# Optimization experiments

Measured on AMD Instinct MI355X. Metric: run time of the kernel, lower is better.

Reference implementation:

```python
import jax, jax.numpy as jnp
from jax import lax
import numpy as np

N_FFT = 1024
HOP = 256
CUTOFF = N_FFT // 2 + 1  # 513


def _make_bases():
    n = np.arange(N_FFT)
    # periodic hann window (scipy get_window('hann', N, fftbins=True))
    win = 0.5 - 0.5 * np.cos(2.0 * np.pi * n / N_FFT)
    fb = np.fft.fft(np.eye(N_FFT))
    FB = np.vstack([fb[:CUTOFF].real, fb[:CUTOFF].imag])  # [1026, 1024]
    scale = N_FFT / HOP
    fwd = (FB * win[None, :]).astype(np.float32)                      # [1026, 1024]
    inv = (np.linalg.pinv(scale * FB).T * win[None, :]).astype(np.float32)  # [1026, 1024]
    win_sq = (win ** 2).astype(np.float32)
    return jnp.asarray(fwd), jnp.asarray(inv), jnp.asarray(win_sq)

FWD_BASIS, INV_BASIS, WIN_SQ = _make_bases()


def setup_inputs() -> dict:
    key = jax.random.key(0)
    k1, k2 = jax.random.split(key)
    audio = jax.random.normal(k1, (4, 1048576), dtype=jnp.float32)
    bias_spec = jax.random.uniform(k2, (1, CUTOFF, 1), dtype=jnp.float32)
    return {"audio": audio, "bias_spec": bias_spec}


def reference(audio, bias_spec):
    strength = 0.1
    pad = N_FFT // 2
    # ---- STFT.transform: reflect pad + strided conv1d with fourier basis ----
    x = jnp.pad(audio, ((0, 0), (pad, pad)), mode='reflect')[:, None, :]  # [B,1,T+N]
    ft = lax.conv_general_dilated(
        x, FWD_BASIS[:, None, :], window_strides=(HOP,), padding='VALID',
        dimension_numbers=('NCH', 'OIH', 'NCH'))  # [B, 1026, F]
    re, im = ft[:, :CUTOFF, :], ft[:, CUTOFF:, :]
    mag = jnp.sqrt(re * re + im * im)
    phase = jnp.arctan2(im, re)
    # ---- denoise: bias subtract + clamp ----
    mag_d = jnp.maximum(mag - bias_spec * strength, 0.0)
    # ---- STFT.inverse: cos/sin recombine + conv_transpose1d ----
    rec = jnp.concatenate([mag_d * jnp.cos(phase), mag_d * jnp.sin(phase)], axis=1)  # [B,1026,F]
    # conv_transpose1d(stride=HOP) == dilated conv with flipped, channel-swapped kernel
    K = jnp.flip(INV_BASIS, axis=-1)[None, :, :]  # OIH: [1, 1026, 1024]
    inv = lax.conv_general_dilated(
        rec, K, window_strides=(1,), padding=[(N_FFT - 1, N_FFT - 1)],
        lhs_dilation=(HOP,), dimension_numbers=('NCH', 'OIH', 'NCH'))  # [B,1,(F-1)*HOP+N]
    # ---- window_sumsquare (vectorized overlap-add of win_sq) ----
    F = mag.shape[-1]
    n_len = N_FFT + HOP * (F - 1)
    idx = (jnp.arange(F)[:, None] * HOP + jnp.arange(N_FFT)[None, :]).reshape(-1)
    ws = jnp.zeros((n_len,), jnp.float32).at[idx].add(jnp.tile(WIN_SQ, F))
    tiny = jnp.finfo(jnp.float32).tiny
    inv = jnp.where(ws > tiny, inv / ws, inv) * (float(N_FFT) / HOP)
    # trim filter_length/2 from both ends
    return inv[:, :, pad:-pad]
```

## Files before the change

kernel.cpp:

```cpp
#include <hip/hip_runtime.h>
#include <math.h>


#define NFFT 1024
#define HOP  256
#define CUT  513
#define NB   4
#define LAUD 1048576
#define NFR  4097
#define NSEG 4224
#define NZROW 4100
#define NCOL 4096
#define ABLEN 1082368

typedef __attribute__((ext_vector_type(4))) float f32x4;
typedef __attribute__((ext_vector_type(8))) short bf16x8;

#define AS1 __attribute__((address_space(1)))
#define AS3 __attribute__((address_space(3)))

__device__ __forceinline__ unsigned short f2bf(float x) {
    unsigned u = __float_as_uint(x);
    u += 0x7FFF + ((u >> 16) & 1);
    return (unsigned short)(u >> 16);
}
__device__ __forceinline__ float bf2f(unsigned short h) {
    return __uint_as_float(((unsigned)h) << 16);
}

__global__ __launch_bounds__(256) void build_bases_k(
    ushort* __restrict__ fwdT, ushort* __restrict__ invT2) {
    __shared__ float ctab[1024];
    const int tid = threadIdx.x, bx = blockIdx.x;
    const float CST = 6.135923151542565e-3f;
    #pragma unroll
    for (int i = 0; i < 4; ++i) ctab[(i << 8) + tid] = cosf(CST * (float)((i << 8) + tid));
    __syncthreads();
    int idx = (bx << 8) + tid;
    {
        int ch = idx >> 8, h = idx & 255;
        int k = (ch < CUT) ? ch : ch - 512;
        int m = (k * h) & 1023;
        float base = (ch < CUT) ? ctab[m] : -ctab[(m + 768) & 1023];
        fwdT[idx] = f2bf(base);
    }
    {
        int h = idx >> 10, ch = idx & 1023;
        int k = (ch < CUT) ? ch : ch - 512;
        int m = (k * h) & 1023;
        float base = (ch < CUT) ? ctab[m] : -ctab[(m + 768) & 1023];
        float d = (k == 0 || k == 512) ? (1.0f / 1024.0f) : (2.0f / 1024.0f);
        invT2[idx] = f2bf(base * d);
    }
}

__global__ void cvt_audio_k(const float* __restrict__ audio, ushort* __restrict__ aud) {
    const int NV = ABLEN / 8;
    int idx = blockIdx.x * blockDim.x + threadIdx.x;
    if (idx >= NB * NV) return;
    int b = idx / NV;
    int t8 = (idx - b * NV) << 3;
    const float* ap = audio + (long)b * LAUD;
    ushort o[8];
    int j0 = t8 - 512;
    if (j0 >= 0 && j0 + 7 < LAUD) {
        f32x4 v0 = *(const f32x4*)(ap + j0);
        f32x4 v1 = *(const f32x4*)(ap + j0 + 4);
        #pragma unroll
        for (int q = 0; q < 4; ++q) { o[q] = f2bf(v0[q]); o[4 + q] = f2bf(v1[q]); }
    } else {
        #pragma unroll
        for (int q = 0; q < 8; ++q) {
            int t = t8 + q;
            float v = 0.f;
            if (t < LAUD + 1024) {
                int j = t - 512;
                if (j < 0) j = -j;
                if (j >= LAUD) j = 2 * LAUD - 2 - j;
                v = ap[j];
            }
            o[q] = f2bf(v);
        }
    }
    *(ushort4*)(aud + (long)b * ABLEN + t8)     = *(ushort4*)&o[0];
    *(ushort4*)(aud + (long)b * ABLEN + t8 + 4) = *(ushort4*)&o[4];
}

__global__ __launch_bounds__(256) void gemm_t_k(
    const ushort* __restrict__ fwdT, const ushort* __restrict__ aud,
    ushort* __restrict__ T) {
    __shared__ char smem[32768];
    const int tid = threadIdx.x;
    const int wid = tid >> 6, lane = tid & 63;
    const int lh = lane & 15, lg = lane >> 4;
    const int wm = wid >> 1, wn = wid & 1;
    int w = (blockIdx.x & 7) * 132 + (blockIdx.x >> 3);
    const int f0 = (w % 33) << 7;
    const int c0 = ((w / 33) & 7) << 7;
    const int b  = w / 264;
    const ushort* ab = aud + (long)b * ABLEN;
    f32x4 acc[4][4] = {};

    for (int k0 = 0; k0 < 256; k0 += 64) {
        if (k0) __syncthreads();
        #pragma unroll
        for (int i = 0; i < 4; ++i) {
            int ci = (i << 8) + tid;
            int row = ci >> 3;
            int ks = k0 + (((ci & 7) ^ (row & 7)) << 3);
            __builtin_amdgcn_global_load_lds(
                (const AS1 unsigned int*)(fwdT + ((c0 + row) << 8) + ks),
                (AS3 unsigned int*)(smem + (i << 12) + (wid << 10)), 16, 0, 0);
            __builtin_amdgcn_global_load_lds(
                (const AS1 unsigned int*)(ab + (f0 + row) * 256 + ks),
                (AS3 unsigned int*)(smem + 16384 + (i << 12) + (wid << 10)), 16, 0, 0);
        }
        __syncthreads();
        #pragma unroll
        for (int s = 0; s < 2; ++s) {
            bf16x8 av[4], bv[4];
            #pragma unroll
            for (int i = 0; i < 4; ++i) {
                int r = (wm << 6) + (i << 4) + lh;
                av[i] = *(const bf16x8*)(smem + (r << 7) + ((((s << 2) + lg) ^ (r & 7)) << 4));
                int q = (wn << 6) + (i << 4) + lh;
                bv[i] = *(const bf16x8*)(smem + 16384 + (q << 7) + ((((s << 2) + lg) ^ (q & 7)) << 4));
            }
            #pragma unroll
            for (int i = 0; i < 4; ++i)
                #pragma unroll
                for (int j = 0; j < 4; ++j)
                    acc[i][j] = __builtin_amdgcn_mfma_f32_16x16x32_bf16(av[i], bv[j], acc[i][j], 0, 0, 0);
        }
    }
    ushort* Tb = T + (long)b * NSEG * 1024;
    #pragma unroll
    for (int i = 0; i < 4; ++i) {
        int c = c0 + (wm << 6) + (i << 4) + (lg << 2);
        #pragma unroll
        for (int j = 0; j < 4; ++j) {
            int g = f0 + (wn << 6) + (j << 4) + lh;
            ushort4 o;
            o.x = f2bf(acc[i][j][0]); o.y = f2bf(acc[i][j][1]);
            o.z = f2bf(acc[i][j][2]); o.w = f2bf(acc[i][j][3]);
            *(ushort4*)(Tb + ((long)g << 10) + c) = o;
        }
    }
}

__global__ __launch_bounds__(256) void elem_a_k(
    const ushort* __restrict__ T, const float* __restrict__ bias,
    ushort* __restrict__ Z) {
    __shared__ ushort Tl[4096];
    __shared__ float Xr[513], Xi[513];
    __shared__ float Zr_[513], Zi_[513];
    int bid = blockIdx.x;
    int b = bid / NFR, f = bid - b * NFR;
    const ushort* Tr = T + ((long)(b * NSEG + f) << 10);
    ushort* Zo = Z + ((long)(b * NZROW + f) << 10);
    const int tid = threadIdx.x;

    ((uint4*)Tl)[tid]       = ((const uint4*)Tr)[tid];
    ((uint4*)Tl)[tid + 256] = ((const uint4*)Tr)[tid + 256];
    __syncthreads();

    #pragma unroll
    for (int half = 0; half < 2; ++half) {
        int k = (half << 8) + tid;
        if (k > 512) continue;
        float a[4], bb[4];
        #pragma unroll
        for (int d = 0; d < 4; ++d) {
            a[d]  = bf2f(Tl[(d << 10) + k]);
            bb[d] = (k >= 1 && k <= 511) ? bf2f(Tl[(d << 10) + 512 + k]) : 0.f;
        }
        int r = k & 3;
        float xr, xi;
        if      (r == 0) { xr = a[0] + a[1] + a[2] + a[3];   xi = bb[0] + bb[1] + bb[2] + bb[3]; }
        else if (r == 1) { xr = a[0] + bb[1] - a[2] - bb[3]; xi = bb[0] - a[1] - bb[2] + a[3]; }
        else if (r == 2) { xr = a[0] - a[1] + a[2] - a[3];   xi = bb[0] - bb[1] + bb[2] - bb[3]; }
        else             { xr = a[0] - bb[1] - a[2] + bb[3]; xi = bb[0] + a[1] - bb[2] - a[3]; }
        Xr[k] = xr; Xi[k] = xi;
    }
    if (tid == 0) {
        float a[4];
        #pragma unroll
        for (int d = 0; d < 4; ++d) a[d] = bf2f(Tl[(d << 10) + 512]);
        Xr[512] = a[0] - a[1] + a[2] - a[3];
        Xr[512] = a[0] + a[1] + a[2] + a[3];
        Xi[512] = 0.f;
    }
    __syncthreads();

    #pragma unroll
    for (int half = 0; half < 3; ++half) {
        int k = (half < 2) ? (half << 8) + tid : 512;
        if (half == 2 && tid != 0) continue;
        if (k > 512) continue;
        int km = k - 1, kp = k + 1;
        float smr, smi, spr, spi;
        if (km < 0) { smr = Xr[1];  smi = -Xi[1]; }  else { smr = Xr[km]; smi = Xi[km]; }
        if (kp > 512) { spr = Xr[511]; spi = -Xi[511]; } else { spr = Xr[kp]; spi = Xi[kp]; }
        float xwr = 0.5f * Xr[k] - 0.25f * (smr + spr);
        float xwi = 0.5f * Xi[k] - 0.25f * (smi + spi);
        float mag = sqrtf(xwr * xwr + xwi * xwi);
        float s = mag > 0.f ? fmaxf(mag - 0.1f * bias[k], 0.f) / mag : 0.f;
        Zr_[k] = xwr * s; Zi_[k] = xwi * s;
    }
    __syncthreads();

    #pragma unroll
    for (int half = 0; half < 3; ++half) {
        int k = (half < 2) ? (half << 8) + tid : 512;
        if (half == 2 && tid != 0) continue;
        if (k > 512) continue;
        int km = k - 1, kp = k + 1;
        float smr, smi, spr, spi;
        if (km < 0) { smr = Zr_[1];  smi = -Zi_[1]; }  else { smr = Zr_[km]; smi = Zi_[km]; }
        if (kp > 512) { spr = Zr_[511]; spi = -Zi_[511]; } else { spr = Zr_[kp]; spi = Zi_[kp]; }
        float zr = 0.5f * Zr_[k] - 0.25f * (smr + spr);
        float zi = 0.5f * Zi_[k] - 0.25f * (smi + spi);
        Zo[k] = f2bf(zr);
        if (k >= 1 && k <= 511) Zo[512 + k] = f2bf(zi);
    }
}

__global__ __launch_bounds__(256) void elem_b_k(
    const ushort* __restrict__ Z, ushort* __restrict__ C) {
    __shared__ ushort Zl[4096];
    int bid = blockIdx.x;
    int b = bid >> 12, j = bid & 4095;
    int g = j + 2;
    const ushort* Zb = Z + (long)b * NZROW * 1024;
    ushort* Cr = C + ((long)(b * NCOL + j) << 10);
    const int tid = threadIdx.x;
    const int f0 = g - 3;

    #pragma unroll
    for (int v = 0; v < 2; ++v) {
        int idx = (v << 8) + tid;
        int row = idx >> 7;
        int f = f0 + row;
        uint4 val = make_uint4(0, 0, 0, 0);
        if (f >= 0 && f < NFR)
            val = ((const uint4*)(Zb + ((long)f << 10)))[idx & 127];
        ((uint4*)Zl)[idx] = val;
    }
    __syncthreads();

    #pragma unroll
    for (int half = 0; half < 3; ++half) {
        int k = (half < 2) ? (half << 8) + tid : 512;
        if (half == 2 && tid != 0) continue;
        if (k > 512) continue;
        int r = k & 3;
        float cr = 0.f, ci = 0.f;
        #pragma unroll
        for (int d = 0; d < 4; ++d) {
            int row = 3 - d;
            float zr = bf2f(Zl[(row << 10) + k]);
            float zi = (k >= 1 && k <= 511) ? bf2f(Zl[(row << 10) + 512 + k]) : 0.f;
            int rd = (d * r) & 3;
            if      (rd == 0) { cr += zr; ci += zi; }
            else if (rd == 1) { cr -= zi; ci += zr; }
            else if (rd == 2) { cr -= zr; ci -= zi; }
            else              { cr += zi; ci -= zr; }
        }
        Cr[k] = f2bf(cr);
        if (k >= 1 && k <= 511) Cr[512 + k] = f2bf(ci);
    }
}

__global__ __launch_bounds__(512) void gemm_c_k(
    const ushort* __restrict__ invT2, const ushort* __restrict__ C,
    float* __restrict__ out) {
    __shared__ char smem[49152];
    const int tid = threadIdx.x;
    const int wid = tid >> 6, lane = tid & 63;
    const int lh = lane & 15, lg = lane >> 4;
    const int g = wid >> 2;
    const int wid2 = wid & 3;
    const int wm = wid2 >> 1, wn = wid2 & 1;
    const int tg = tid & 255;
    int w = (blockIdx.x & 7) * 64 + (blockIdx.x >> 3);
    const int h0  = (w & 1) << 7;
    const int j0  = ((w >> 1) & 63) << 6;
    const int fo0 = 2 + j0;
    const int b   = w >> 7;
    const ushort* Cb = C + (long)b * NCOL * 1024;
    char* sm = smem + g * 24576;
    f32x4 acc[4][2] = {};

    for (int k0s = 0; k0s < 512; k0s += 64) {
        if (k0s) __syncthreads();
        int kk = (g << 9) + k0s;
        #pragma unroll
        for (int i = 0; i < 4; ++i) {
            int ci = (i << 8) + tg;
            int row = ci >> 3;
            int swz = (((ci & 7) ^ (row & 7)) << 3);
            __builtin_amdgcn_global_load_lds(
                (const AS1 unsigned int*)(invT2 + ((h0 + row) << 10) + kk + swz),
                (AS3 unsigned int*)(sm + (i << 12) + (wid2 << 10)), 16, 0, 0);
        }
        #pragma unroll
        for (int i = 0; i < 2; ++i) {
            int ci = (i << 8) + tg;
            int row = ci >> 3;
            int swz = (((ci & 7) ^ (row & 7)) << 3);
            __builtin_amdgcn_global_load_lds(
                (const AS1 unsigned int*)(Cb + ((long)(j0 + row) << 10) + kk + swz),
                (AS3 unsigned int*)(sm + 16384 + (i << 12) + (wid2 << 10)), 16, 0, 0);
        }
        __syncthreads();
        #pragma unroll
        for (int s = 0; s < 2; ++s) {
            bf16x8 av[4], bv[2];
            #pragma unroll
            for (int i = 0; i < 4; ++i) {
                int r = (wm << 6) + (i << 4) + lh;
                av[i] = *(const bf16x8*)(sm + (r << 7) + ((((s << 2) + lg) ^ (r & 7)) << 4));
            }
            #pragma unroll
            for (int j = 0; j < 2; ++j) {
                int rq = (wn << 5) + (j << 4) + lh;
                bv[j] = *(const bf16x8*)(sm + 16384 + (rq << 7) + ((((s << 2) + lg) ^ (rq & 7)) << 4));
            }
            #pragma unroll
            for (int i = 0; i < 4; ++i)
                #pragma unroll
                for (int j = 0; j < 2; ++j)
                    acc[i][j] = __builtin_amdgcn_mfma_f32_16x16x32_bf16(av[i], bv[j], acc[i][j], 0, 0, 0);
        }
    }
    __syncthreads();
    float* red = (float*)smem;
    if (g == 1) {
        #pragma unroll
        for (int i = 0; i < 4; ++i)
            #pragma unroll
            for (int j = 0; j < 2; ++j) {
                int hl = (wm << 6) + (i << 4) + (lg << 2);
                int fl = (wn << 5) + (j << 4) + lh;
                #pragma unroll
                for (int q = 0; q < 4; ++q)
                    red[(hl + q) * 64 + fl] = acc[i][j][q];
            }
    }
    __syncthreads();
    if (g == 1) return;
    float* ob = out + (long)b * LAUD;
    const float CST = 6.135923151542565e-3f;
    #pragma unroll
    for (int i = 0; i < 4; ++i) {
        int hbase = h0 + (wm << 6) + (i << 4) + (lg << 2);
        int hl = (wm << 6) + (i << 4) + (lg << 2);
        #pragma unroll
        for (int j = 0; j < 2; ++j) {
            int fo = fo0 + (wn << 5) + (j << 4) + lh;
            int fl = (wn << 5) + (j << 4) + lh;
            f32x4 v = acc[i][j];
            #pragma unroll
            for (int q = 0; q < 4; ++q) v[q] += red[(hl + q) * 64 + fl];
            if (fo == 2 || fo == 4097) {
                #pragma unroll
                for (int q = 0; q < 4; ++q) {
                    int n = (fo == 2) ? (hbase + q + 768) : (hbase + q);
                    float w2 = 0.5f - 0.5f * cosf(CST * (float)n);
                    v[q] = v[q] * (1.0f / (1.5f - w2 * w2));
                }
            } else {
                v *= (2.0f / 3.0f);
            }
            *(f32x4*)(ob + (((long)(fo - 2)) << 8) + hbase) = v;
        }
    }
}

extern "C" void kernel_launch(void* const* d_in, const int* in_sizes, int n_in,
                              void* d_out, int out_size, void* d_ws, size_t ws_size,
                              hipStream_t stream) {
    const float* audio = (const float*)d_in[0];
    const float* bias  = (const float*)d_in[1];
    float* out = (float*)d_out;
    char* wsb = (char*)d_ws;

    ushort* fwdT  = (ushort*)(wsb);
    ushort* invT2 = (ushort*)(wsb + 524288);
    ushort* aud   = (ushort*)(wsb + 1048576);
    ushort* T     = (ushort*)(wsb + 9707520);
    ushort* Z     = (ushort*)(wsb + 44310528);
    ushort* C     = (ushort*)(wsb + 77897728);

    build_bases_k<<<1024, 256, 0, stream>>>(fwdT, invT2);

    int cvt_total = NB * (ABLEN / 8);
    cvt_audio_k<<<(cvt_total + 255) / 256, 256, 0, stream>>>(audio, aud);

    gemm_t_k<<<1056, 256, 0, stream>>>(fwdT, aud, T);

    elem_a_k<<<NB * NFR, 256, 0, stream>>>(T, bias, Z);

    elem_b_k<<<NB * NCOL, 256, 0, stream>>>(Z, C);

    gemm_c_k<<<512, 512, 0, stream>>>(invT2, C, out);
}
```

Baseline: 116.2 us.

## Process eight frames per block in elementwise kernels to reuse overlapping rows

After: 115.8 us. No clear change (-0.4%).

```diff
diff --git a/kernel.cpp b/kernel.cpp
--- a/kernel.cpp
+++ b/kernel.cpp
@@ -151,123 +151,136 @@
 __global__ __launch_bounds__(256) void elem_a_k(
     const ushort* __restrict__ T, const float* __restrict__ bias,
     ushort* __restrict__ Z) {
-    __shared__ ushort Tl[4096];
-    __shared__ float Xr[513], Xi[513];
-    __shared__ float Zr_[513], Zi_[513];
+    __shared__ ushort Tl[11 * 1024];
+    __shared__ float Xr[513], Xi[513], Zr_[513], Zi_[513];
     int bid = blockIdx.x;
-    int b = bid / NFR, f = bid - b * NFR;
-    const ushort* Tr = T + ((long)(b * NSEG + f) << 10);
-    ushort* Zo = Z + ((long)(b * NZROW + f) << 10);
+    int x = bid & 7, s = bid >> 3;
+    int w = (x < 4) ? x * 257 + s : 1028 + (x - 4) * 256 + s;
+    int b = w / 513, fblk = w - b * 513;
+    int f0 = fblk << 3;
+    const ushort* Tb = T + (long)b * NSEG * 1024;
+    ushort* Zb = Z + (long)b * NZROW * 1024;
     const int tid = threadIdx.x;
 
-    ((uint4*)Tl)[tid]       = ((const uint4*)Tr)[tid];
-    ((uint4*)Tl)[tid + 256] = ((const uint4*)Tr)[tid + 256];
+    const uint4* src = (const uint4*)(Tb + ((long)f0 << 10));
+    #pragma unroll
+    for (int i = 0; i < 6; ++i) {
+        int idx = (i << 8) + tid;
+        if (idx < 1408) ((uint4*)Tl)[idx] = src[idx];
+    }
     __syncthreads();
 
-    #pragma unroll
-    for (int half = 0; half < 2; ++half) {
-        int k = (half << 8) + tid;
-        if (k > 512) continue;
-        float a[4], bb[4];
-        #pragma unroll
-        for (int d = 0; d < 4; ++d) {
-            a[d]  = bf2f(Tl[(d << 10) + k]);
-            bb[d] = (k >= 1 && k <= 511) ? bf2f(Tl[(d << 10) + 512 + k]) : 0.f;
-        }
-        int r = k & 3;
-        float xr, xi;
-        if      (r == 0) { xr = a[0] + a[1] + a[2] + a[3];   xi = bb[0] + bb[1] + bb[2] + bb[3]; }
-        else if (r == 1) { xr = a[0] + bb[1] - a[2] - bb[3]; xi = bb[0] - a[1] - bb[2] + a[3]; }
-        else if (r == 2) { xr = a[0] - a[1] + a[2] - a[3];   xi = bb[0] - bb[1] + bb[2] - bb[3]; }
-        else             { xr = a[0] - bb[1] - a[2] + bb[3]; xi = bb[0] + a[1] - bb[2] - a[3]; }
-        Xr[k] = xr; Xi[k] = xi;
-    }
-    if (tid == 0) {
-        float a[4];
-        #pragma unroll
-        for (int d = 0; d < 4; ++d) a[d] = bf2f(Tl[(d << 10) + 512]);
-        Xr[512] = a[0] - a[1] + a[2] - a[3];
-        Xr[512] = a[0] + a[1] + a[2] + a[3];
-        Xi[512] = 0.f;
-    }
-    __syncthreads();
-
-    #pragma unroll
-    for (int half = 0; half < 3; ++half) {
-        int k = (half < 2) ? (half << 8) + tid : 512;
-        if (half == 2 && tid != 0) continue;
-        if (k > 512) continue;
-        int km = k - 1, kp = k + 1;
-        float smr, smi, spr, spi;
-        if (km < 0) { smr = Xr[1];  smi = -Xi[1]; }  else { smr = Xr[km]; smi = Xi[km]; }
-        if (kp > 512) { spr = Xr[511]; spi = -Xi[511]; } else { spr = Xr[kp]; spi = Xi[kp]; }
-        float xwr = 0.5f * Xr[k] - 0.25f * (smr + spr);
-        float xwi = 0.5f * Xi[k] - 0.25f * (smi + spi);
-        float mag = sqrtf(xwr * xwr + xwi * xwi);
-        float s = mag > 0.f ? fmaxf(mag - 0.1f * bias[k], 0.f) / mag : 0.f;
-        Zr_[k] = xwr * s; Zi_[k] = xwi * s;
-    }
-    __syncthreads();
-
-    #pragma unroll
-    for (int half = 0; half < 3; ++half) {
-        int k = (half < 2) ? (half << 8) + tid : 512;
-        if (half == 2 && tid != 0) continue;
-        if (k > 512) continue;
-        int km = k - 1, kp = k + 1;
-        float smr, smi, spr, spi;
-        if (km < 0) { smr = Zr_[1];  smi = -Zi_[1]; }  else { smr = Zr_[km]; smi = Zi_[km]; }
-        if (kp > 512) { spr = Zr_[511]; spi = -Zi_[511]; } else { spr = Zr_[kp]; spi = Zi_[kp]; }
-        float zr = 0.5f * Zr_[k] - 0.25f * (smr + spr);
-        float zi = 0.5f * Zi_[k] - 0.25f * (smi + spi);
-        Zo[k] = f2bf(zr);
-        if (k >= 1 && k <= 511) Zo[512 + k] = f2bf(zi);
+    for (int fi = 0; fi < 8; ++fi) {
+        int f = f0 + fi;
+        if (f >= NFR) break;
+        #pragma unroll
+        for (int half = 0; half < 2; ++half) {
+            int k = (half << 8) + tid;
+            float a[4], bb[4];
+            #pragma unroll
+            for (int d = 0; d < 4; ++d) {
+                a[d]  = bf2f(Tl[((fi + d) << 10) + k]);
+                bb[d] = (k >= 1) ? bf2f(Tl[((fi + d) << 10) + 512 + k]) : 0.f;
+            }
+            int r = k & 3;
+            float xr, xi;
+            if      (r == 0) { xr = a[0] + a[1] + a[2] + a[3];   xi = bb[0] + bb[1] + bb[2] + bb[3]; }
+            else if (r == 1) { xr = a[0] + bb[1] - a[2] - bb[3]; xi = bb[0] - a[1] - bb[2] + a[3]; }
+            else if (r == 2) { xr = a[0] - a[1] + a[2] - a[3];   xi = bb[0] - bb[1] + bb[2] - bb[3]; }
+            else             { xr = a[0] - bb[1] - a[2] + bb[3]; xi = bb[0] + a[1] - bb[2] - a[3]; }
+            Xr[k] = xr; Xi[k] = xi;
+        }
+        if (tid == 0) {
+            Xr[512] = bf2f(Tl[(fi << 10) + 512]) + bf2f(Tl[((fi + 1) << 10) + 512])
+                    + bf2f(Tl[((fi + 2) << 10) + 512]) + bf2f(Tl[((fi + 3) << 10) + 512]);
+            Xi[512] = 0.f;
+        }
+        __syncthreads();
+        #pragma unroll
+        for (int half = 0; half < 3; ++half) {
+            int k = (half < 2) ? (half << 8) + tid : 512;
+            if (half == 2 && tid != 0) continue;
+            int km = k - 1, kp = k + 1;
+            float smr, smi, spr, spi;
+            if (km < 0)   { smr = Xr[1];   smi = -Xi[1]; }   else { smr = Xr[km]; smi = Xi[km]; }
+            if (kp > 512) { spr = Xr[511]; spi = -Xi[511]; } else { spr = Xr[kp]; spi = Xi[kp]; }
+            float xwr = 0.5f * Xr[k] - 0.25f * (smr + spr);
+            float xwi = 0.5f * Xi[k] - 0.25f * (smi + spi);
+            float mag = sqrtf(xwr * xwr + xwi * xwi);
+            float sc = mag > 0.f ? fmaxf(mag - 0.1f * bias[k], 0.f) / mag : 0.f;
+            Zr_[k] = xwr * sc; Zi_[k] = xwi * sc;
+        }
+        __syncthreads();
+        ushort* Zo = Zb + ((long)f << 10);
+        #pragma unroll
+        for (int half = 0; half < 3; ++half) {
+            int k = (half < 2) ? (half << 8) + tid : 512;
+            if (half == 2 && tid != 0) continue;
+            int km = k - 1, kp = k + 1;
+            float smr, smi, spr, spi;
+            if (km < 0)   { smr = Zr_[1];   smi = -Zi_[1]; }   else { smr = Zr_[km]; smi = Zi_[km]; }
+            if (kp > 512) { spr = Zr_[511]; spi = -Zi_[511]; } else { spr = Zr_[kp]; spi = Zi_[kp]; }
+            float zr = 0.5f * Zr_[k] - 0.25f * (smr + spr);
+            float zi = 0.5f * Zi_[k] - 0.25f * (smi + spi);
+            Zo[k] = f2bf(zr);
+            if (k >= 1 && k <= 511) Zo[512 + k] = f2bf(zi);
+        }
+        __syncthreads();
     }
 }
 
 __global__ __launch_bounds__(256) void elem_b_k(
     const ushort* __restrict__ Z, ushort* __restrict__ C) {
-    __shared__ ushort Zl[4096];
+    __shared__ ushort Zl[11 * 1024];
     int bid = blockIdx.x;
-    int b = bid >> 12, j = bid & 4095;
-    int g = j + 2;
+    int w = (bid & 7) * 256 + (bid >> 3);
+    int b = w >> 9, gblk = w & 511;
+    int g0 = 2 + (gblk << 3);
     const ushort* Zb = Z + (long)b * NZROW * 1024;
-    ushort* Cr = C + ((long)(b * NCOL + j) << 10);
+    ushort* Cb = C + (long)b * NCOL * 1024;
     const int tid = threadIdx.x;
-    const int f0 = g - 3;
+    const int fbase = g0 - 3;
 
     #pragma unroll
-    for (int v = 0; v < 2; ++v) {
-        int idx = (v << 8) + tid;
-        int row = idx >> 7;
-        int f = f0 + row;
-        uint4 val = make_uint4(0, 0, 0, 0);
-        if (f >= 0 && f < NFR)
-            val = ((const uint4*)(Zb + ((long)f << 10)))[idx & 127];
-        ((uint4*)Zl)[idx] = val;
+    for (int i = 0; i < 6; ++i) {
+        int idx = (i << 8) + tid;
+        if (idx < 1408) {
+            int row = idx >> 7;
+            int f = fbase + row;
+            uint4 v = make_uint4(0, 0, 0, 0);
+            if (f >= 0 && f < NFR)
+                v = ((const uint4*)(Zb + ((long)f << 10)))[idx & 127];
+            ((uint4*)Zl)[idx] = v;
+        }
     }
     __syncthreads();
 
-    #pragma unroll
-    for (int half = 0; half < 3; ++half) {
-        int k = (half < 2) ? (half << 8) + tid : 512;
-        if (half == 2 && tid != 0) continue;
-        if (k > 512) continue;
-        int r = k & 3;
-        float cr = 0.f, ci = 0.f;
-        #pragma unroll
-        for (int d = 0; d < 4; ++d) {
-            int row = 3 - d;
-            float zr = bf2f(Zl[(row << 10) + k]);
-            float zi = (k >= 1 && k <= 511) ? bf2f(Zl[(row << 10) + 512 + k]) : 0.f;
-            int rd = (d * r) & 3;
-            if      (rd == 0) { cr += zr; ci += zi; }
-            else if (rd == 1) { cr -= zi; ci += zr; }
-            else if (rd == 2) { cr -= zr; ci -= zi; }
-            else              { cr += zi; ci -= zr; }
-        }
-        Cr[k] = f2bf(cr);
-        if (k >= 1 && k <= 511) Cr[512 + k] = f2bf(ci);
+    for (int gi = 0; gi < 8; ++gi) {
+        ushort* Cr = Cb + ((long)(g0 + gi - 2) << 10);
+        #pragma unroll
+        for (int half = 0; half < 2; ++half) {
+            int k = (half << 8) + tid;
+            int r = k & 3;
+            float cr = 0.f, ci = 0.f;
+            #pragma unroll
+            for (int d = 0; d < 4; ++d) {
+                int row = gi + 3 - d;
+                float zr = bf2f(Zl[(row << 10) + k]);
+                float zi = (k >= 1) ? bf2f(Zl[(row << 10) + 512 + k]) : 0.f;
+                int rd = (d * r) & 3;
+                if      (rd == 0) { cr += zr; ci += zi; }
+                else if (rd == 1) { cr -= zi; ci += zr; }
+                else if (rd == 2) { cr -= zr; ci -= zi; }
+                else              { cr += zi; ci -= zr; }
+            }
+            Cr[k] = f2bf(cr);
+            if (k >= 1) Cr[512 + k] = f2bf(ci);
+        }
+        if (tid == 0) {
+            float cr = bf2f(Zl[((gi + 3) << 10) + 512]) + bf2f(Zl[((gi + 2) << 10) + 512])
+                     + bf2f(Zl[((gi + 1) << 10) + 512]) + bf2f(Zl[(gi << 10) + 512]);
+            Cr[512] = f2bf(cr);
+        }
     }
 }
 
@@ -399,9 +412,9 @@
 
     gemm_t_k<<<1056, 256, 0, stream>>>(fwdT, aud, T);
 
-    elem_a_k<<<NB * NFR, 256, 0, stream>>>(T, bias, Z);
-
-    elem_b_k<<<NB * NCOL, 256, 0, stream>>>(Z, C);
+    elem_a_k<<<2052, 256, 0, stream>>>(T, bias, Z);
+
+    elem_b_k<<<2048, 256, 0, stream>>>(Z, C);
 
     gemm_c_k<<<512, 512, 0, stream>>>(invT2, C, out);
 }
```
